# Kernel tuning notes

Hardware: AMD Instinct MI355X
Metric: run time of the kernel (lower is better)

## Reference

```python
import jax, jax.numpy as jnp
from jax import lax
import numpy as np

VOCAB, EMB = 50000, 300
HID, NCLS = 100, 20
BATCH, SEQ = 128, 512
P_DROP = 0.5


def setup_inputs() -> dict:
    key = jax.random.key(0)
    ks = jax.random.split(key, 8)
    s_e = 1.0 / np.sqrt(EMB)
    s_h = 1.0 / np.sqrt(HID)
    return {
        "inputs_batch": jax.random.randint(ks[0], (BATCH, SEQ), 0, VOCAB, dtype=jnp.int64)
        if jax.config.jax_enable_x64 else jax.random.randint(ks[0], (BATCH, SEQ), 0, VOCAB, dtype=jnp.int32),
        "emb_table": jax.random.normal(ks[1], (VOCAB, EMB), dtype=jnp.float32),
        # GRUCell params (torch layout): gates order [r, z, n]
        "w_ih": jax.random.uniform(ks[2], (3 * HID, EMB), jnp.float32, -s_h, s_h),
        "w_hh": jax.random.uniform(ks[3], (3 * HID, HID), jnp.float32, -s_h, s_h),
        "b_ih": jax.random.uniform(ks[4], (3 * HID,), jnp.float32, -s_h, s_h),
        "b_hh": jax.random.uniform(ks[5], (3 * HID,), jnp.float32, -s_h, s_h),
        "w_lin": jax.random.uniform(ks[6], (NCLS, HID), jnp.float32, -s_h, s_h),
        "b_lin": jax.random.uniform(ks[7], (NCLS,), jnp.float32, -s_h, s_h),
    }


def reference(inputs_batch, emb_table, w_ih, w_hh, b_ih, b_hh, w_lin, b_lin):
    B, S = inputs_batch.shape
    H = w_hh.shape[1]
    keep = 1.0 - P_DROP
    dk1, dk2 = jax.random.split(jax.random.key(42))

    z_embed = emb_table[inputs_batch]                       # [B, S, E]
    m1 = jax.random.bernoulli(dk1, keep, z_embed.shape)     # dropout1 mask
    z_embed = jnp.where(m1, z_embed / keep, 0.0)
    x_seq = jnp.swapaxes(z_embed, 0, 1)                     # [S, B, E]
    m2 = jax.random.bernoulli(dk2, keep, (S, B, H))         # per-step dropout2 masks

    def step(h, inp):
        x, m = inp
        gi = x @ w_ih.T + b_ih                              # [B, 3H]
        gh = h @ w_hh.T + b_hh
        i_r, i_z, i_n = jnp.split(gi, 3, axis=-1)
        h_r, h_z, h_n = jnp.split(gh, 3, axis=-1)
        r = jax.nn.sigmoid(i_r + h_r)
        zg = jax.nn.sigmoid(i_z + h_z)
        n = jnp.tanh(i_n + r * h_n)
        h_new = (1.0 - zg) * n + zg * h
        h_d = jnp.where(m, h_new / keep, 0.0)
        y = jax.nn.log_softmax(h_d @ w_lin.T + b_lin, axis=1)  # [B, C]
        return h_new, y

    h0 = jnp.zeros((B, H), dtype=x_seq.dtype)
    _, ys = lax.scan(step, h0, (x_seq, m2))                 # ys: [S, B, C]
    return jnp.transpose(ys, (1, 2, 0))                     # [B, C, S]
```

## Files before the change

kernel.cpp:

```cpp
#include <hip/hip_runtime.h>
#include <hip/hip_bf16.h>
#include <cstdint>

#define BATCH 128
#define SEQ   512
#define EMB   300
#define HID   100
#define G3    300
#define NCLS  20
#define NROWS (SEQ * BATCH)

#define M1_WORDS 614400
#define M2_WORDS 204800

typedef __attribute__((ext_vector_type(4))) float f32x4;
typedef __attribute__((ext_vector_type(8))) short s16x8;
typedef __fp16 h16x2 __attribute__((ext_vector_type(2)));

__host__ __device__ __forceinline__ void threefry2x32(uint32_t k0, uint32_t k1,
                                                      uint32_t x0, uint32_t x1,
                                                      uint32_t* o0, uint32_t* o1) {
  uint32_t ks2 = k0 ^ k1 ^ 0x1BD11BDAu;
  x0 += k0; x1 += k1;
#define TFR(r) { x0 += x1; x1 = (x1 << (r)) | (x1 >> (32 - (r))); x1 ^= x0; }
  TFR(13) TFR(15) TFR(26) TFR(6)  x0 += k1;  x1 += ks2 + 1u;
  TFR(17) TFR(29) TFR(16) TFR(24) x0 += ks2; x1 += k0 + 2u;
  TFR(13) TFR(15) TFR(26) TFR(6)  x0 += k0;  x1 += k1 + 3u;
  TFR(17) TFR(29) TFR(16) TFR(24) x0 += k1;  x1 += ks2 + 4u;
  TFR(13) TFR(15) TFR(26) TFR(6)  x0 += ks2; x1 += k0 + 5u;
#undef TFR
  *o0 = x0; *o1 = x1;
}

__device__ __forceinline__ uint32_t rand_bits32(uint32_t ka, uint32_t kb, uint32_t flat) {
  uint32_t a, b;
  threefry2x32(ka, kb, 0u, flat, &a, &b);
  return a ^ b;
}

__device__ __forceinline__ short f2bf(float f) {
  union { float f; uint32_t u; } c; c.f = f;
  uint32_t u = c.u;
  return (short)((u + 0x7FFFu + ((u >> 16) & 1u)) >> 16);
}

__device__ __forceinline__ void bar_lds() {
  __asm__ __volatile__("s_waitcnt lgkmcnt(0)" ::: "memory");
  __builtin_amdgcn_s_barrier();
  __asm__ __volatile__("" ::: "memory");
}

__device__ __forceinline__ float swz_xor4(float x) {
  return __builtin_bit_cast(float,
      __builtin_amdgcn_ds_swizzle(__builtin_bit_cast(int, x), 0x101F));
}

__global__ __launch_bounds__(256) void k_mask(uint32_t* __restrict__ M1w,
                                              uint32_t* __restrict__ M2w,
                                              uint32_t k1a, uint32_t k1b,
                                              uint32_t k2a, uint32_t k2b) {
  const int i = blockIdx.x * 256 + threadIdx.x;
  uint32_t ka, kb, base;
  uint32_t* dst;
  if (i < M1_WORDS) { ka = k1a; kb = k1b; base = (uint32_t)i * 32u; dst = M1w + i; }
  else { ka = k2a; kb = k2b; base = (uint32_t)(i - M1_WORDS) * 32u; dst = M2w + (i - M1_WORDS); }
  uint32_t w = 0u;
#pragma unroll
  for (int j = 0; j < 32; ++j) {
    uint32_t bits = rand_bits32(ka, kb, base + (uint32_t)j);
    w |= ((~bits) >> 31) << j;
  }
  *dst = w;
}

__global__ __launch_bounds__(256) void k_prepw(const float* __restrict__ w_ih,
                                               short* __restrict__ Wb) {
  int i8 = (blockIdx.x * 256 + threadIdx.x) * 8;
  if (i8 >= 304 * 320) return;
  short o[8];
#pragma unroll
  for (int j = 0; j < 8; ++j) {
    int pos = i8 + j;
    int n = pos / 320, k = pos - (pos / 320) * 320;
    float v = (n < 300 && k < 300) ? w_ih[(size_t)n * EMB + k] : 0.f;
    o[j] = f2bf(v);
  }
  *(s16x8*)(Wb + i8) = *(s16x8*)o;
}

__global__ __launch_bounds__(512) void k_gi7(const int* __restrict__ inputs,
                                             const float* __restrict__ emb,
                                             const short* __restrict__ Wb,
                                             const float* __restrict__ b_ih,
                                             const uint32_t* __restrict__ M1w,
                                             float* __restrict__ GI) {
  __shared__ short As[128 * 40];
  __shared__ short Bs[304 * 40];
  __shared__ int idxs[128];
  const int t = threadIdx.x;
  const int s = blockIdx.x;
  const int lane = t & 63, wave = t >> 6;
  const int wr = wave & 1;
  const int wc = wave >> 1;
  const int ml = lane & 15, quad = lane >> 4;
  const int arow = t >> 2;
  const int akq = t & 3;

  if (t < 128) idxs[t] = inputs[t * SEQ + s];
  __syncthreads();

  const int nfr = (wc < 3) ? 5 : 4;
  f32x4 acc[4][5];
#pragma unroll
  for (int i = 0; i < 4; ++i)
#pragma unroll
    for (int j = 0; j < 5; ++j) acc[i][j] = (f32x4){0.f, 0.f, 0.f, 0.f};

  const int myidx = idxs[arow];

  for (int c = 0; c < 10; ++c) {
    const int e0 = c * 32 + akq * 8;
    float xa[8];
#pragma unroll
    for (int j = 0; j < 8; ++j) xa[j] = 0.f;
    if (e0 + 7 < 300) {
#pragma unroll
      for (int q4 = 0; q4 < 2; ++q4) {
        float4 v = *(const float4*)(emb + (size_t)myidx * EMB + e0 + q4 * 4);
        xa[q4 * 4 + 0] = v.x; xa[q4 * 4 + 1] = v.y; xa[q4 * 4 + 2] = v.z; xa[q4 * 4 + 3] = v.w;
      }
    } else if (e0 < 300) {
#pragma unroll
      for (int j = 0; j < 8; ++j) {
        int e = e0 + j;
        if (e < 300) xa[j] = emb[(size_t)myidx * EMB + e];
      }
    }
    uint32_t mb = 0;
    if (e0 < 300) {
      uint32_t base = (uint32_t)((arow * SEQ + s) * EMB + e0);
      uint64_t mw = (uint64_t)M1w[base >> 5] | ((uint64_t)M1w[(base >> 5) + 1] << 32);
      mb = (uint32_t)(mw >> (base & 31));
    }
    short sa[8];
#pragma unroll
    for (int j = 0; j < 8; ++j)
      sa[j] = f2bf(((mb >> j) & 1u) ? xa[j] * 2.f : 0.f);
    s16x8 bv0, bv1, bv2;
    {
      int i0 = t;
      bv0 = *(const s16x8*)(Wb + (size_t)(i0 >> 2) * 320 + c * 32 + (i0 & 3) * 8);
      int i1 = t + 512;
      bv1 = *(const s16x8*)(Wb + (size_t)(i1 >> 2) * 320 + c * 32 + (i1 & 3) * 8);
      if (t < 192) {
        int i2 = t + 1024;
        bv2 = *(const s16x8*)(Wb + (size_t)(i2 >> 2) * 320 + c * 32 + (i2 & 3) * 8);
      }
    }
    if (c > 0) __syncthreads();
    *(s16x8*)&As[arow * 40 + akq * 8] = *(s16x8*)&sa[0];
    {
      int i0 = t;       *(s16x8*)&Bs[(i0 >> 2) * 40 + (i0 & 3) * 8] = bv0;
      int i1 = t + 512; *(s16x8*)&Bs[(i1 >> 2) * 40 + (i1 & 3) * 8] = bv1;
      if (t < 192) { int i2 = t + 1024; *(s16x8*)&Bs[(i2 >> 2) * 40 + (i2 & 3) * 8] = bv2; }
    }
    __syncthreads();
    s16x8 af[4];
#pragma unroll
    for (int mt = 0; mt < 4; ++mt)
      af[mt] = *(const s16x8*)&As[(wr * 64 + mt * 16 + ml) * 40 + quad * 8];
#pragma unroll
    for (int j = 0; j < 5; ++j) {
      if (j < nfr) {
        int nt = wc + 4 * j;
        s16x8 bf = *(const s16x8*)&Bs[(nt * 16 + ml) * 40 + quad * 8];
#pragma unroll
        for (int mt = 0; mt < 4; ++mt)
          acc[mt][j] = __builtin_amdgcn_mfma_f32_16x16x32_bf16(af[mt], bf, acc[mt][j], 0, 0, 0);
      }
    }
  }

#pragma unroll
  for (int j = 0; j < 5; ++j) {
    if (j < nfr) {
      int n = (wc + 4 * j) * 16 + ml;
      if (n < 300) {
        float bias = b_ih[n];
#pragma unroll
        for (int mt = 0; mt < 4; ++mt) {
#pragma unroll
          for (int i = 0; i < 4; ++i) {
            int brow = wr * 64 + mt * 16 + quad * 4 + i;
            GI[(size_t)(s * BATCH + brow) * G3 + n] = acc[mt][j][i] + bias;
          }
        }
      }
    }
  }
}

__global__ __launch_bounds__(512, 1) void k_rnn11(const float* __restrict__ GI,
                                                  const float* __restrict__ w_hh,
                                                  const float* __restrict__ b_hh,
                                                  const uint8_t* __restrict__ M2,
                                                  float* __restrict__ Hd) {
  __shared__ __align__(16) uint32_t hp_s[2][64];
  const int t = threadIdx.x, b = blockIdx.x;
  const int u = t >> 2, ks = t & 3;
  const bool act = (u < 100);
  const bool gate = act && (ks == 0);
  const int uc = act ? u : 99;
  const int kplo = (ks < 2) ? ks * 13 : 26 + (ks - 2) * 12;
  const int np = (ks < 2) ? 13 : 12;

  const float* rowR = w_hh + (size_t)uc * HID;
  const float* rowZ = w_hh + (size_t)(uc + 100) * HID;
  const float* rowN = w_hh + (size_t)(uc + 200) * HID;
  const h16x2 z2 = (h16x2){(__fp16)0.f, (__fp16)0.f};
  h16x2 wR[13], wZ[13], wN[13];
#pragma unroll
  for (int j = 0; j < 13; ++j) {
    if (j < np) {
      int o = 2 * (kplo + j);
      wR[j] = __builtin_amdgcn_cvt_pkrtz(rowR[o], rowR[o + 1]);
      wZ[j] = __builtin_amdgcn_cvt_pkrtz(rowZ[o], rowZ[o + 1]);
      wN[j] = __builtin_amdgcn_cvt_pkrtz(rowN[o], rowN[o + 1]);
    } else { wR[j] = z2; wZ[j] = z2; wN[j] = z2; }
  }

  float bR0 = 0.f, bZ0 = 0.f, bN0 = 0.f;
  float gcR = 0.f, gcZ = 0.f, gcN = 0.f;
  uint8_t mc = 0;
  if (gate) {
    bR0 = b_hh[u]; bZ0 = b_hh[100 + u]; bN0 = b_hh[200 + u];
    const float* g0 = GI + (size_t)b * G3;
    gcR = g0[u]; gcZ = g0[100 + u]; gcN = g0[200 + u];
    mc = M2[(uint32_t)(b * HID + u) >> 3];
  }
  const int p = u >> 1;
  const int sidx = (p < 13) ? 0 : (p < 26) ? 1 : (p < 38) ? 2 : 3;
  const int spos = p - ((sidx < 2) ? sidx * 13 : 26 + (sidx - 2) * 12);
  const int slot = sidx * 16 + spos;
  const bool writer = gate && !(u & 1);

  if (t < 128) ((uint32_t*)hp_s)[t] = 0u;
  float hprev = 0.f;
  __syncthreads();

#define QPX(x, c) __builtin_bit_cast(float, __builtin_amdgcn_mov_dpp( \
    __builtin_bit_cast(int, (x)), (c), 0xF, 0xF, true))
#define DOT1(J, W) { h16x2 hh = __builtin_bit_cast(h16x2, (W)); \
    sR = __builtin_amdgcn_fdot2(wR[J], hh, sR, false); \
    sZ = __builtin_amdgcn_fdot2(wZ[J], hh, sZ, false); \
    sN = __builtin_amdgcn_fdot2(wN[J], hh, sN, false); }

#pragma unroll 2
  for (int s = 0; s < SEQ; ++s) {
    float gnR = 0.f, gnZ = 0.f, gnN = 0.f;
    uint8_t mn = 0;
    if (gate) {
      int sn = (s + 1 < SEQ) ? s + 1 : s;
      const float* gp = GI + (size_t)(sn * BATCH + b) * G3;
      gnR = gp[u]; gnZ = gp[100 + u]; gnN = gp[200 + u];
      mn = M2[(uint32_t)((sn * BATCH + b) * HID + u) >> 3];
    }
    if (act) {
      float sR = bR0, sZ = bZ0, sN = bN0;
      const uint32_t* hb = &hp_s[s & 1][0] + (ks << 4);
      uint4 h0 = *(const uint4*)hb;
      uint4 h1 = *(const uint4*)(hb + 4);
      uint4 h2 = *(const uint4*)(hb + 8);
      uint32_t h3 = hb[12];
      DOT1(0, h0.x)  DOT1(1, h0.y)  DOT1(2, h0.z)  DOT1(3, h0.w)
      DOT1(4, h1.x)  DOT1(5, h1.y)  DOT1(6, h1.z)  DOT1(7, h1.w)
      DOT1(8, h2.x)  DOT1(9, h2.y)  DOT1(10, h2.z) DOT1(11, h2.w)
      DOT1(12, h3)
      sR += QPX(sR, 0xB1); sZ += QPX(sZ, 0xB1); sN += QPX(sN, 0xB1);
      sR += QPX(sR, 0x4E); sZ += QPX(sZ, 0x4E); sN += QPX(sN, 0x4E);
      if (gate) {
        float r = 1.f / (1.f + __expf(-(gcR + sR)));
        float z = 1.f / (1.f + __expf(-(gcZ + sZ)));
        float xn = gcN + r * sN;
        float e2 = __expf(2.f * fabsf(xn));
        float n = copysignf(1.f - 2.f / (e2 + 1.f), xn);
        float hnew = (1.f - z) * n + z * hprev;
        hprev = hnew;
        uint32_t fl = (uint32_t)((s * BATCH + b) * HID + u);
        float hd = ((mc >> (fl & 7)) & 1u) ? hnew * 2.f : 0.f;
        Hd[(size_t)(b * SEQ + s) * HID + u] = hd;
        float hoth = swz_xor4(hnew);
        if (writer)
          hp_s[(s & 1) ^ 1][slot] =
              __builtin_bit_cast(uint32_t, __builtin_amdgcn_cvt_pkrtz(hnew, hoth));
      }
    }
    gcR = gnR; gcZ = gnZ; gcN = gnN; mc = mn;
    bar_lds();
  }
#undef DOT1
#undef QPX
}

__global__ __launch_bounds__(64) void k_out(const float* __restrict__ Hd,
                                            const float* __restrict__ w_lin,
                                            const float* __restrict__ b_lin,
                                            float* __restrict__ out) {
  __shared__ float Wl[NCLS * HID];
  __shared__ float bl[NCLS];
  const int t = threadIdx.x;
  for (int i = t; i < NCLS * HID; i += 64) Wl[i] = w_lin[i];
  if (t < NCLS) bl[t] = b_lin[t];
  __syncthreads();

  const int r0 = (blockIdx.x * 64 + t) * 4;
  float acc[4][NCLS];
#pragma unroll
  for (int r = 0; r < 4; ++r)
#pragma unroll
    for (int c = 0; c < NCLS; ++c) acc[r][c] = bl[c];

  for (int k = 0; k < HID; k += 4) {
    float4 h0 = *(const float4*)(Hd + (size_t)(r0 + 0) * HID + k);
    float4 h1 = *(const float4*)(Hd + (size_t)(r0 + 1) * HID + k);
    float4 h2 = *(const float4*)(Hd + (size_t)(r0 + 2) * HID + k);
    float4 h3 = *(const float4*)(Hd + (size_t)(r0 + 3) * HID + k);
#pragma unroll
    for (int c = 0; c < NCLS; ++c) {
      float4 w4 = *(const float4*)&Wl[c * HID + k];
      acc[0][c] += h0.x * w4.x + h0.y * w4.y + h0.z * w4.z + h0.w * w4.w;
      acc[1][c] += h1.x * w4.x + h1.y * w4.y + h1.z * w4.z + h1.w * w4.w;
      acc[2][c] += h2.x * w4.x + h2.y * w4.y + h2.z * w4.z + h2.w * w4.w;
      acc[3][c] += h3.x * w4.x + h3.y * w4.y + h3.z * w4.z + h3.w * w4.w;
    }
  }

  float lse[4];
#pragma unroll
  for (int r = 0; r < 4; ++r) {
    float mx = acc[r][0];
#pragma unroll
    for (int c = 1; c < NCLS; ++c) mx = fmaxf(mx, acc[r][c]);
    float se = 0.f;
#pragma unroll
    for (int c = 0; c < NCLS; ++c) se += __expf(acc[r][c] - mx);
    lse[r] = mx + __logf(se);
  }
  const int b = r0 >> 9, s0 = r0 & 511;
#pragma unroll
  for (int c = 0; c < NCLS; ++c) {
    float4 o = make_float4(acc[0][c] - lse[0], acc[1][c] - lse[1],
                           acc[2][c] - lse[2], acc[3][c] - lse[3]);
    *(float4*)(out + (size_t)(b * NCLS + c) * SEQ + s0) = o;
  }
}

extern "C" void kernel_launch(void* const* d_in, const int* in_sizes, int n_in,
                              void* d_out, int out_size, void* d_ws, size_t ws_size,
                              hipStream_t stream) {
  const int*   inputs = (const int*)d_in[0];
  const float* emb    = (const float*)d_in[1];
  const float* w_ih   = (const float*)d_in[2];
  const float* w_hh   = (const float*)d_in[3];
  const float* b_ih   = (const float*)d_in[4];
  const float* b_hh   = (const float*)d_in[5];
  const float* w_lin  = (const float*)d_in[6];
  const float* b_lin  = (const float*)d_in[7];
  float* out = (float*)d_out;

  float* GI = (float*)d_ws;
  float* Hd = GI + (size_t)NROWS * G3;
  uint8_t* M1 = (uint8_t*)(Hd + (size_t)NROWS * HID);
  uint8_t* M2 = M1 + (size_t)M1_WORDS * 4;
  short* Wb = (short*)(M2 + (size_t)M2_WORDS * 4);

  uint32_t dk1a, dk1b, dk2a, dk2b;
  threefry2x32(0u, 42u, 0u, 0u, &dk1a, &dk1b);
  threefry2x32(0u, 42u, 0u, 1u, &dk2a, &dk2b);

  k_mask<<<(M1_WORDS + M2_WORDS) / 256, 256, 0, stream>>>(
      (uint32_t*)M1, (uint32_t*)M2, dk1a, dk1b, dk2a, dk2b);
  k_prepw<<<(304 * 320 / 8 + 255) / 256, 256, 0, stream>>>(w_ih, Wb);
  k_gi7<<<512, 512, 0, stream>>>(inputs, emb, Wb, b_ih, (const uint32_t*)M1, GI);
  k_rnn11<<<BATCH, 512, 0, stream>>>(GI, w_hh, b_hh, M2, Hd);
  k_out<<<256, 64, 0, stream>>>(Hd, w_lin, b_lin, out);
}
```

Baseline: 557.7 us.

## Split embedding gather and dropout into separate bf16 pre-pass before GI GEMM

```diff
diff --git a/kernel.cpp b/kernel.cpp
--- a/kernel.cpp
+++ b/kernel.cpp
@@ -86,6 +86,122 @@
     o[j] = f2bf(v);
   }
   *(s16x8*)(Wb + i8) = *(s16x8*)o;
+}
+
+__global__ __launch_bounds__(256) void k_prepx(const int* __restrict__ inputs,
+                                               const float* __restrict__ emb,
+                                               const uint32_t* __restrict__ M1w,
+                                               short* __restrict__ Xb) {
+  const int i8 = blockIdx.x * 256 + threadIdx.x;
+  const int r = i8 / 40, c8 = i8 - r * 40;
+  const int e = c8 * 8;
+  const int b = r & 127, sq = r >> 7;
+  short o[8];
+  if (e >= 300) {
+#pragma unroll
+    for (int j = 0; j < 8; ++j) o[j] = 0;
+  } else {
+    const int tok = inputs[b * SEQ + sq];
+    const float* er = emb + (size_t)tok * EMB + e;
+    float xa[8];
+    if (e + 8 <= 300) {
+      float4 v0 = *(const float4*)(er);
+      float4 v1 = *(const float4*)(er + 4);
+      xa[0] = v0.x; xa[1] = v0.y; xa[2] = v0.z; xa[3] = v0.w;
+      xa[4] = v1.x; xa[5] = v1.y; xa[6] = v1.z; xa[7] = v1.w;
+    } else {
+      float4 v0 = *(const float4*)(er);
+      xa[0] = v0.x; xa[1] = v0.y; xa[2] = v0.z; xa[3] = v0.w;
+      xa[4] = xa[5] = xa[6] = xa[7] = 0.f;
+    }
+    const uint32_t flat = (uint32_t)((b * SEQ + sq) * EMB + e);
+    uint64_t mw = (uint64_t)M1w[flat >> 5] | ((uint64_t)M1w[(flat >> 5) + 1] << 32);
+    uint32_t mb = (uint32_t)(mw >> (flat & 31));
+#pragma unroll
+    for (int j = 0; j < 8; ++j)
+      o[j] = f2bf(((mb >> j) & 1u) ? xa[j] * 2.f : 0.f);
+  }
+  *(s16x8*)(Xb + (size_t)i8 * 8) = *(s16x8*)o;
+}
+
+__global__ __launch_bounds__(512) void k_gi8(const short* __restrict__ Xb,
+                                             const short* __restrict__ Wb,
+                                             const float* __restrict__ b_ih,
+                                             float* __restrict__ GI) {
+  __shared__ short As[128 * 40];
+  __shared__ short Bs[304 * 40];
+  const int t = threadIdx.x;
+  const int s = blockIdx.x;
+  const int lane = t & 63, wave = t >> 6;
+  const int wr = wave & 1;
+  const int wc = wave >> 1;
+  const int ml = lane & 15, quad = lane >> 4;
+  const int arow = t >> 2;
+  const int akq = t & 3;
+
+  const int nfr = (wc < 3) ? 5 : 4;
+  f32x4 acc[4][5];
+#pragma unroll
+  for (int i = 0; i < 4; ++i)
+#pragma unroll
+    for (int j = 0; j < 5; ++j) acc[i][j] = (f32x4){0.f, 0.f, 0.f, 0.f};
+
+  const short* xrow = Xb + ((size_t)(s * 128) + arow) * 320;
+
+  for (int c = 0; c < 10; ++c) {
+    s16x8 av = *(const s16x8*)(xrow + c * 32 + akq * 8);
+    s16x8 bv0, bv1, bv2;
+    {
+      int i0 = t;
+      bv0 = *(const s16x8*)(Wb + (size_t)(i0 >> 2) * 320 + c * 32 + (i0 & 3) * 8);
+      int i1 = t + 512;
+      bv1 = *(const s16x8*)(Wb + (size_t)(i1 >> 2) * 320 + c * 32 + (i1 & 3) * 8);
+      if (t < 192) {
+        int i2 = t + 1024;
+        bv2 = *(const s16x8*)(Wb + (size_t)(i2 >> 2) * 320 + c * 32 + (i2 & 3) * 8);
+      }
+    }
+    if (c > 0) __syncthreads();
+    *(s16x8*)&As[arow * 40 + akq * 8] = av;
+    {
+      int i0 = t;       *(s16x8*)&Bs[(i0 >> 2) * 40 + (i0 & 3) * 8] = bv0;
+      int i1 = t + 512; *(s16x8*)&Bs[(i1 >> 2) * 40 + (i1 & 3) * 8] = bv1;
+      if (t < 192) { int i2 = t + 1024; *(s16x8*)&Bs[(i2 >> 2) * 40 + (i2 & 3) * 8] = bv2; }
+    }
+    __syncthreads();
+    s16x8 af[4];
+#pragma unroll
+    for (int mt = 0; mt < 4; ++mt)
+      af[mt] = *(const s16x8*)&As[(wr * 64 + mt * 16 + ml) * 40 + quad * 8];
+#pragma unroll
+    for (int j = 0; j < 5; ++j) {
+      if (j < nfr) {
+        int nt = wc + 4 * j;
+        s16x8 bf = *(const s16x8*)&Bs[(nt * 16 + ml) * 40 + quad * 8];
+#pragma unroll
+        for (int mt = 0; mt < 4; ++mt)
+          acc[mt][j] = __builtin_amdgcn_mfma_f32_16x16x32_bf16(af[mt], bf, acc[mt][j], 0, 0, 0);
+      }
+    }
+  }
+
+#pragma unroll
+  for (int j = 0; j < 5; ++j) {
+    if (j < nfr) {
+      int n = (wc + 4 * j) * 16 + ml;
+      if (n < 300) {
+        float bias = b_ih[n];
+#pragma unroll
+        for (int mt = 0; mt < 4; ++mt) {
+#pragma unroll
+          for (int i = 0; i < 4; ++i) {
+            int brow = wr * 64 + mt * 16 + quad * 4 + i;
+            GI[(size_t)(s * BATCH + brow) * G3 + n] = acc[mt][j][i] + bias;
+          }
+        }
+      }
+    }
+  }
 }
 
 __global__ __launch_bounds__(512) void k_gi7(const int* __restrict__ inputs,
@@ -265,6 +381,7 @@
       gnR = gp[u]; gnZ = gp[100 + u]; gnN = gp[200 + u];
       mn = M2[(uint32_t)((sn * BATCH + b) * HID + u) >> 3];
     }
+
     if (act) {
       float sR = bR0, sZ = bZ0, sN = bN0;
       const uint32_t* hb = &hp_s[s & 1][0] + (ks << 4);
@@ -287,7 +404,7 @@
         float hnew = (1.f - z) * n + z * hprev;
         hprev = hnew;
         uint32_t fl = (uint32_t)((s * BATCH + b) * HID + u);
-        float hd = ((mc >> (fl & 7)) & 1u) ? hnew * 2.f : 0.f;
+        float hd = ((mc >> (fl & 7)) & 1) ? hnew * 2.f : 0.f;
         Hd[(size_t)(b * SEQ + s) * HID + u] = hd;
         float hoth = swz_xor4(hnew);
         if (writer)
@@ -373,6 +490,8 @@
   uint8_t* M1 = (uint8_t*)(Hd + (size_t)NROWS * HID);
   uint8_t* M2 = M1 + (size_t)M1_WORDS * 4;
   short* Wb = (short*)(M2 + (size_t)M2_WORDS * 4);
+  short* Xb = Wb + 304 * 320;
+  const size_t need_xb = 150272000;
 
   uint32_t dk1a, dk1b, dk2a, dk2b;
   threefry2x32(0u, 42u, 0u, 0u, &dk1a, &dk1b);
@@ -381,7 +500,13 @@
   k_mask<<<(M1_WORDS + M2_WORDS) / 256, 256, 0, stream>>>(
       (uint32_t*)M1, (uint32_t*)M2, dk1a, dk1b, dk2a, dk2b);
   k_prepw<<<(304 * 320 / 8 + 255) / 256, 256, 0, stream>>>(w_ih, Wb);
-  k_gi7<<<512, 512, 0, stream>>>(inputs, emb, Wb, b_ih, (const uint32_t*)M1, GI);
+  if (ws_size >= need_xb) {
+    k_prepx<<<65536 * 40 / 256, 256, 0, stream>>>(inputs, emb,
+                                                  (const uint32_t*)M1, Xb);
+    k_gi8<<<512, 512, 0, stream>>>(Xb, Wb, b_ih, GI);
+  } else {
+    k_gi7<<<512, 512, 0, stream>>>(inputs, emb, Wb, b_ih, (const uint32_t*)M1, GI);
+  }
   k_rnn11<<<BATCH, 512, 0, stream>>>(GI, w_hh, b_hh, M2, Hd);
   k_out<<<256, 64, 0, stream>>>(Hd, w_lin, b_lin, out);
 }
```

New measurement: 559.4 us. About the same (+0.3%).

## Fuse input projection, GRU recurrence and output head into one per-batch kernel

Applied to the files above, without the earlier changes.

```diff
diff --git a/kernel.cpp b/kernel.cpp
--- a/kernel.cpp
+++ b/kernel.cpp
@@ -55,198 +55,209 @@
       __builtin_amdgcn_ds_swizzle(__builtin_bit_cast(int, x), 0x101F));
 }
 
-__global__ __launch_bounds__(256) void k_mask(uint32_t* __restrict__ M1w,
+__global__ __launch_bounds__(256) void k_prep(uint32_t* __restrict__ M1w,
                                               uint32_t* __restrict__ M2w,
+                                              const float* __restrict__ w_ih,
+                                              short* __restrict__ Wb,
                                               uint32_t k1a, uint32_t k1b,
                                               uint32_t k2a, uint32_t k2b) {
-  const int i = blockIdx.x * 256 + threadIdx.x;
-  uint32_t ka, kb, base;
-  uint32_t* dst;
-  if (i < M1_WORDS) { ka = k1a; kb = k1b; base = (uint32_t)i * 32u; dst = M1w + i; }
-  else { ka = k2a; kb = k2b; base = (uint32_t)(i - M1_WORDS) * 32u; dst = M2w + (i - M1_WORDS); }
-  uint32_t w = 0u;
-#pragma unroll
-  for (int j = 0; j < 32; ++j) {
-    uint32_t bits = rand_bits32(ka, kb, base + (uint32_t)j);
-    w |= ((~bits) >> 31) << j;
+  const int bid = blockIdx.x;
+  if (bid < 3200) {
+    const int i = bid * 256 + threadIdx.x;
+    uint32_t ka, kb, base;
+    uint32_t* dst;
+    if (i < M1_WORDS) { ka = k1a; kb = k1b; base = (uint32_t)i * 32u; dst = M1w + i; }
+    else { ka = k2a; kb = k2b; base = (uint32_t)(i - M1_WORDS) * 32u; dst = M2w + (i - M1_WORDS); }
+    uint32_t w = 0u;
+#pragma unroll
+    for (int j = 0; j < 32; ++j) {
+      uint32_t bits = rand_bits32(ka, kb, base + (uint32_t)j);
+      w |= ((~bits) >> 31) << j;
+    }
+    *dst = w;
+  } else {
+    int i8 = ((bid - 3200) * 256 + threadIdx.x) * 8;
+    if (i8 >= 304 * 320) return;
+    short o[8];
+#pragma unroll
+    for (int j = 0; j < 8; ++j) {
+      int pos = i8 + j;
+      int n = pos / 320, k = pos - (pos / 320) * 320;
+      float v = (n < 300 && k < 300) ? w_ih[(size_t)n * EMB + k] : 0.f;
+      o[j] = f2bf(v);
+    }
+    *(s16x8*)(Wb + i8) = *(s16x8*)o;
   }
-  *dst = w;
-}
-
-__global__ __launch_bounds__(256) void k_prepw(const float* __restrict__ w_ih,
-                                               short* __restrict__ Wb) {
-  int i8 = (blockIdx.x * 256 + threadIdx.x) * 8;
-  if (i8 >= 304 * 320) return;
-  short o[8];
-#pragma unroll
-  for (int j = 0; j < 8; ++j) {
-    int pos = i8 + j;
-    int n = pos / 320, k = pos - (pos / 320) * 320;
-    float v = (n < 300 && k < 300) ? w_ih[(size_t)n * EMB + k] : 0.f;
-    o[j] = f2bf(v);
+}
+
+__global__ __launch_bounds__(512, 1) void k_main(const int* __restrict__ inputs,
+                                                 const float* __restrict__ emb,
+                                                 const short* __restrict__ Wb,
+                                                 const float* __restrict__ b_ih,
+                                                 const uint32_t* __restrict__ M1w,
+                                                 float* __restrict__ GI,
+                                                 const float* __restrict__ w_hh,
+                                                 const float* __restrict__ b_hh,
+                                                 const uint8_t* __restrict__ M2,
+                                                 float* __restrict__ Hd,
+                                                 const float* __restrict__ w_lin,
+                                                 const float* __restrict__ b_lin,
+                                                 float* __restrict__ out) {
+  __shared__ __align__(16) char smem[35072];
+  const int t = threadIdx.x, b = blockIdx.x;
+  float* GIb = GI + (size_t)b * SEQ * G3;
+
+  {
+    short* As = (short*)smem;
+    short* Bs = As + 128 * 40;
+    int* idxs = (int*)(Bs + 304 * 40);
+    const int lane = t & 63, wave = t >> 6;
+    const int wr = wave & 1, wc = wave >> 1;
+    const int ml = lane & 15, quad = lane >> 4;
+    const int arow = t >> 2, akq = t & 3;
+    const int nfr = (wc < 3) ? 5 : 4;
+
+    for (int tile = 0; tile < 4; ++tile) {
+      __syncthreads();
+      if (t < 128) idxs[t] = inputs[b * SEQ + tile * 128 + t];
+      __syncthreads();
+
+      f32x4 acc[4][5];
+#pragma unroll
+      for (int i = 0; i < 4; ++i)
+#pragma unroll
+        for (int j = 0; j < 5; ++j) acc[i][j] = (f32x4){0.f, 0.f, 0.f, 0.f};
+
+      const int myidx = idxs[arow];
+      const int srow = tile * 128 + arow;
+
+      for (int c = 0; c < 10; ++c) {
+        const int e0 = c * 32 + akq * 8;
+        float xa[8];
+#pragma unroll
+        for (int j = 0; j < 8; ++j) xa[j] = 0.f;
+        if (e0 + 7 < 300) {
+#pragma unroll
+          for (int q4 = 0; q4 < 2; ++q4) {
+            float4 v = *(const float4*)(emb + (size_t)myidx * EMB + e0 + q4 * 4);
+            xa[q4 * 4 + 0] = v.x; xa[q4 * 4 + 1] = v.y;
+            xa[q4 * 4 + 2] = v.z; xa[q4 * 4 + 3] = v.w;
+          }
+        } else if (e0 < 300) {
+#pragma unroll
+          for (int j = 0; j < 8; ++j) {
+            int e = e0 + j;
+            if (e < 300) xa[j] = emb[(size_t)myidx * EMB + e];
+          }
+        }
+        uint32_t mb = 0;
+        if (e0 < 300) {
+          uint32_t base = (uint32_t)((b * SEQ + srow) * EMB + e0);
+          uint64_t mw = (uint64_t)M1w[base >> 5] | ((uint64_t)M1w[(base >> 5) + 1] << 32);
+          mb = (uint32_t)(mw >> (base & 31));
+        }
+        short sa[8];
+#pragma unroll
+        for (int j = 0; j < 8; ++j)
+          sa[j] = f2bf(((mb >> j) & 1u) ? xa[j] * 2.f : 0.f);
+        s16x8 bv0, bv1, bv2;
+        {
+          int i0 = t;
+          bv0 = *(const s16x8*)(Wb + (size_t)(i0 >> 2) * 320 + c * 32 + (i0 & 3) * 8);
+          int i1 = t + 512;
+          bv1 = *(const s16x8*)(Wb + (size_t)(i1 >> 2) * 320 + c * 32 + (i1 & 3) * 8);
+          if (t < 192) {
+            int i2 = t + 1024;
+            bv2 = *(const s16x8*)(Wb + (size_t)(i2 >> 2) * 320 + c * 32 + (i2 & 3) * 8);
+          }
+        }
+        if (c > 0) __syncthreads();
+        *(s16x8*)&As[arow * 40 + akq * 8] = *(s16x8*)&sa[0];
+        {
+          int i0 = t;       *(s16x8*)&Bs[(i0 >> 2) * 40 + (i0 & 3) * 8] = bv0;
+          int i1 = t + 512; *(s16x8*)&Bs[(i1 >> 2) * 40 + (i1 & 3) * 8] = bv1;
+          if (t < 192) { int i2 = t + 1024; *(s16x8*)&Bs[(i2 >> 2) * 40 + (i2 & 3) * 8] = bv2; }
+        }
+        __syncthreads();
+        s16x8 af[4];
+#pragma unroll
+        for (int mt = 0; mt < 4; ++mt)
+          af[mt] = *(const s16x8*)&As[(wr * 64 + mt * 16 + ml) * 40 + quad * 8];
+#pragma unroll
+        for (int j = 0; j < 5; ++j) {
+          if (j < nfr) {
+            int nt = wc + 4 * j;
+            s16x8 bf = *(const s16x8*)&Bs[(nt * 16 + ml) * 40 + quad * 8];
+#pragma unroll
+            for (int mt = 0; mt < 4; ++mt)
+              acc[mt][j] = __builtin_amdgcn_mfma_f32_16x16x32_bf16(af[mt], bf, acc[mt][j], 0, 0, 0);
+          }
+        }
+      }
+
+#pragma unroll
+      for (int j = 0; j < 5; ++j) {
+        if (j < nfr) {
+          int n = (wc + 4 * j) * 16 + ml;
+          if (n < 300) {
+            float bias = b_ih[n];
+#pragma unroll
+            for (int mt = 0; mt < 4; ++mt) {
+#pragma unroll
+              for (int i = 0; i < 4; ++i) {
+                int so = tile * 128 + wr * 64 + mt * 16 + quad * 4 + i;
+                GIb[(size_t)so * G3 + n] = acc[mt][j][i] + bias;
+              }
+            }
+          }
+        }
+      }
+    }
   }
-  *(s16x8*)(Wb + i8) = *(s16x8*)o;
-}
-
-__global__ __launch_bounds__(512) void k_gi7(const int* __restrict__ inputs,
-                                             const float* __restrict__ emb,
-                                             const short* __restrict__ Wb,
-                                             const float* __restrict__ b_ih,
-                                             const uint32_t* __restrict__ M1w,
-                                             float* __restrict__ GI) {
-  __shared__ short As[128 * 40];
-  __shared__ short Bs[304 * 40];
-  __shared__ int idxs[128];
-  const int t = threadIdx.x;
-  const int s = blockIdx.x;
-  const int lane = t & 63, wave = t >> 6;
-  const int wr = wave & 1;
-  const int wc = wave >> 1;
-  const int ml = lane & 15, quad = lane >> 4;
-  const int arow = t >> 2;
-  const int akq = t & 3;
-
-  if (t < 128) idxs[t] = inputs[t * SEQ + s];
+  __threadfence_block();
   __syncthreads();
 
-  const int nfr = (wc < 3) ? 5 : 4;
-  f32x4 acc[4][5];
-#pragma unroll
-  for (int i = 0; i < 4; ++i)
-#pragma unroll
-    for (int j = 0; j < 5; ++j) acc[i][j] = (f32x4){0.f, 0.f, 0.f, 0.f};
-
-  const int myidx = idxs[arow];
-
-  for (int c = 0; c < 10; ++c) {
-    const int e0 = c * 32 + akq * 8;
-    float xa[8];
-#pragma unroll
-    for (int j = 0; j < 8; ++j) xa[j] = 0.f;
-    if (e0 + 7 < 300) {
-#pragma unroll
-      for (int q4 = 0; q4 < 2; ++q4) {
-        float4 v = *(const float4*)(emb + (size_t)myidx * EMB + e0 + q4 * 4);
-        xa[q4 * 4 + 0] = v.x; xa[q4 * 4 + 1] = v.y; xa[q4 * 4 + 2] = v.z; xa[q4 * 4 + 3] = v.w;
-      }
-    } else if (e0 < 300) {
-#pragma unroll
-      for (int j = 0; j < 8; ++j) {
-        int e = e0 + j;
-        if (e < 300) xa[j] = emb[(size_t)myidx * EMB + e];
-      }
-    }
-    uint32_t mb = 0;
-    if (e0 < 300) {
-      uint32_t base = (uint32_t)((arow * SEQ + s) * EMB + e0);
-      uint64_t mw = (uint64_t)M1w[base >> 5] | ((uint64_t)M1w[(base >> 5) + 1] << 32);
-      mb = (uint32_t)(mw >> (base & 31));
-    }
-    short sa[8];
-#pragma unroll
-    for (int j = 0; j < 8; ++j)
-      sa[j] = f2bf(((mb >> j) & 1u) ? xa[j] * 2.f : 0.f);
-    s16x8 bv0, bv1, bv2;
-    {
-      int i0 = t;
-      bv0 = *(const s16x8*)(Wb + (size_t)(i0 >> 2) * 320 + c * 32 + (i0 & 3) * 8);
-      int i1 = t + 512;
-      bv1 = *(const s16x8*)(Wb + (size_t)(i1 >> 2) * 320 + c * 32 + (i1 & 3) * 8);
-      if (t < 192) {
-        int i2 = t + 1024;
-        bv2 = *(const s16x8*)(Wb + (size_t)(i2 >> 2) * 320 + c * 32 + (i2 & 3) * 8);
-      }
-    }
-    if (c > 0) __syncthreads();
-    *(s16x8*)&As[arow * 40 + akq * 8] = *(s16x8*)&sa[0];
-    {
-      int i0 = t;       *(s16x8*)&Bs[(i0 >> 2) * 40 + (i0 & 3) * 8] = bv0;
-      int i1 = t + 512; *(s16x8*)&Bs[(i1 >> 2) * 40 + (i1 & 3) * 8] = bv1;
-      if (t < 192) { int i2 = t + 1024; *(s16x8*)&Bs[(i2 >> 2) * 40 + (i2 & 3) * 8] = bv2; }
-    }
+  {
+    uint32_t (*hp_s)[64] = (uint32_t (*)[64])smem;
+    const int u = t >> 2, ks = t & 3;
+    const bool act = (u < 100);
+    const bool gate = act && (ks == 0);
+    const int uc = act ? u : 99;
+    const int kplo = (ks < 2) ? ks * 13 : 26 + (ks - 2) * 12;
+    const int np = (ks < 2) ? 13 : 12;
+
+    const float* rowR = w_hh + (size_t)uc * HID;
+    const float* rowZ = w_hh + (size_t)(uc + 100) * HID;
+    const float* rowN = w_hh + (size_t)(uc + 200) * HID;
+    const h16x2 z2 = (h16x2){(__fp16)0.f, (__fp16)0.f};
+    h16x2 wR[13], wZ[13], wN[13];
+#pragma unroll
+    for (int j = 0; j < 13; ++j) {
+      if (j < np) {
+        int o = 2 * (kplo + j);
+        wR[j] = __builtin_amdgcn_cvt_pkrtz(rowR[o], rowR[o + 1]);
+        wZ[j] = __builtin_amdgcn_cvt_pkrtz(rowZ[o], rowZ[o + 1]);
+        wN[j] = __builtin_amdgcn_cvt_pkrtz(rowN[o], rowN[o + 1]);
+      } else { wR[j] = z2; wZ[j] = z2; wN[j] = z2; }
+    }
+
+    float bR0 = 0.f, bZ0 = 0.f, bN0 = 0.f;
+    float gcR = 0.f, gcZ = 0.f, gcN = 0.f;
+    uint8_t mc = 0;
+    if (gate) {
+      bR0 = b_hh[u]; bZ0 = b_hh[100 + u]; bN0 = b_hh[200 + u];
+      gcR = GIb[u]; gcZ = GIb[100 + u]; gcN = GIb[200 + u];
+      mc = M2[(uint32_t)(b * HID + u) >> 3];
+    }
+    const int p = u >> 1;
+    const int sidx = (p < 13) ? 0 : (p < 26) ? 1 : (p < 38) ? 2 : 3;
+    const int spos = p - ((sidx < 2) ? sidx * 13 : 26 + (sidx - 2) * 12);
+    const int slot = sidx * 16 + spos;
+    const bool writer = gate && !(u & 1);
+
+    if (t < 128) ((uint32_t*)hp_s)[t] = 0u;
+    float hprev = 0.f;
     __syncthreads();
-    s16x8 af[4];
-#pragma unroll
-    for (int mt = 0; mt < 4; ++mt)
-      af[mt] = *(const s16x8*)&As[(wr * 64 + mt * 16 + ml) * 40 + quad * 8];
-#pragma unroll
-    for (int j = 0; j < 5; ++j) {
-      if (j < nfr) {
-        int nt = wc + 4 * j;
-        s16x8 bf = *(const s16x8*)&Bs[(nt * 16 + ml) * 40 + quad * 8];
-#pragma unroll
-        for (int mt = 0; mt < 4; ++mt)
-          acc[mt][j] = __builtin_amdgcn_mfma_f32_16x16x32_bf16(af[mt], bf, acc[mt][j], 0, 0, 0);
-      }
-    }
-  }
-
-#pragma unroll
-  for (int j = 0; j < 5; ++j) {
-    if (j < nfr) {
-      int n = (wc + 4 * j) * 16 + ml;
-      if (n < 300) {
-        float bias = b_ih[n];
-#pragma unroll
-        for (int mt = 0; mt < 4; ++mt) {
-#pragma unroll
-          for (int i = 0; i < 4; ++i) {
-            int brow = wr * 64 + mt * 16 + quad * 4 + i;
-            GI[(size_t)(s * BATCH + brow) * G3 + n] = acc[mt][j][i] + bias;
-          }
-        }
-      }
-    }
-  }
-}
-
-__global__ __launch_bounds__(512, 1) void k_rnn11(const float* __restrict__ GI,
-                                                  const float* __restrict__ w_hh,
-                                                  const float* __restrict__ b_hh,
-                                                  const uint8_t* __restrict__ M2,
-                                                  float* __restrict__ Hd) {
-  __shared__ __align__(16) uint32_t hp_s[2][64];
-  const int t = threadIdx.x, b = blockIdx.x;
-  const int u = t >> 2, ks = t & 3;
-  const bool act = (u < 100);
-  const bool gate = act && (ks == 0);
-  const int uc = act ? u : 99;
-  const int kplo = (ks < 2) ? ks * 13 : 26 + (ks - 2) * 12;
-  const int np = (ks < 2) ? 13 : 12;
-
-  const float* rowR = w_hh + (size_t)uc * HID;
-  const float* rowZ = w_hh + (size_t)(uc + 100) * HID;
-  const float* rowN = w_hh + (size_t)(uc + 200) * HID;
-  const h16x2 z2 = (h16x2){(__fp16)0.f, (__fp16)0.f};
-  h16x2 wR[13], wZ[13], wN[13];
-#pragma unroll
-  for (int j = 0; j < 13; ++j) {
-    if (j < np) {
-      int o = 2 * (kplo + j);
-      wR[j] = __builtin_amdgcn_cvt_pkrtz(rowR[o], rowR[o + 1]);
-      wZ[j] = __builtin_amdgcn_cvt_pkrtz(rowZ[o], rowZ[o + 1]);
-      wN[j] = __builtin_amdgcn_cvt_pkrtz(rowN[o], rowN[o + 1]);
-    } else { wR[j] = z2; wZ[j] = z2; wN[j] = z2; }
-  }
-
-  float bR0 = 0.f, bZ0 = 0.f, bN0 = 0.f;
-  float gcR = 0.f, gcZ = 0.f, gcN = 0.f;
-  uint8_t mc = 0;
-  if (gate) {
-    bR0 = b_hh[u]; bZ0 = b_hh[100 + u]; bN0 = b_hh[200 + u];
-    const float* g0 = GI + (size_t)b * G3;
-    gcR = g0[u]; gcZ = g0[100 + u]; gcN = g0[200 + u];
-    mc = M2[(uint32_t)(b * HID + u) >> 3];
-  }
-  const int p = u >> 1;
-  const int sidx = (p < 13) ? 0 : (p < 26) ? 1 : (p < 38) ? 2 : 3;
-  const int spos = p - ((sidx < 2) ? sidx * 13 : 26 + (sidx - 2) * 12);
-  const int slot = sidx * 16 + spos;
-  const bool writer = gate && !(u & 1);
-
-  if (t < 128) ((uint32_t*)hp_s)[t] = 0u;
-  float hprev = 0.f;
-  __syncthreads();
 
 #define QPX(x, c) __builtin_bit_cast(float, __builtin_amdgcn_mov_dpp( \
     __builtin_bit_cast(int, (x)), (c), 0xF, 0xF, true))
@@ -256,102 +267,84 @@
     sN = __builtin_amdgcn_fdot2(wN[J], hh, sN, false); }
 
 #pragma unroll 2
-  for (int s = 0; s < SEQ; ++s) {
-    float gnR = 0.f, gnZ = 0.f, gnN = 0.f;
-    uint8_t mn = 0;
-    if (gate) {
-      int sn = (s + 1 < SEQ) ? s + 1 : s;
-      const float* gp = GI + (size_t)(sn * BATCH + b) * G3;
-      gnR = gp[u]; gnZ = gp[100 + u]; gnN = gp[200 + u];
-      mn = M2[(uint32_t)((sn * BATCH + b) * HID + u) >> 3];
-    }
-    if (act) {
-      float sR = bR0, sZ = bZ0, sN = bN0;
-      const uint32_t* hb = &hp_s[s & 1][0] + (ks << 4);
-      uint4 h0 = *(const uint4*)hb;
-      uint4 h1 = *(const uint4*)(hb + 4);
-      uint4 h2 = *(const uint4*)(hb + 8);
-      uint32_t h3 = hb[12];
-      DOT1(0, h0.x)  DOT1(1, h0.y)  DOT1(2, h0.z)  DOT1(3, h0.w)
-      DOT1(4, h1.x)  DOT1(5, h1.y)  DOT1(6, h1.z)  DOT1(7, h1.w)
-      DOT1(8, h2.x)  DOT1(9, h2.y)  DOT1(10, h2.z) DOT1(11, h2.w)
-      DOT1(12, h3)
-      sR += QPX(sR, 0xB1); sZ += QPX(sZ, 0xB1); sN += QPX(sN, 0xB1);
-      sR += QPX(sR, 0x4E); sZ += QPX(sZ, 0x4E); sN += QPX(sN, 0x4E);
+    for (int s = 0; s < SEQ; ++s) {
+      float gnR = 0.f, gnZ = 0.f, gnN = 0.f;
+      uint8_t mn = 0;
       if (gate) {
-        float r = 1.f / (1.f + __expf(-(gcR + sR)));
-        float z = 1.f / (1.f + __expf(-(gcZ + sZ)));
-        float xn = gcN + r * sN;
-        float e2 = __expf(2.f * fabsf(xn));
-        float n = copysignf(1.f - 2.f / (e2 + 1.f), xn);
-        float hnew = (1.f - z) * n + z * hprev;
-        hprev = hnew;
-        uint32_t fl = (uint32_t)((s * BATCH + b) * HID + u);
-        float hd = ((mc >> (fl & 7)) & 1u) ? hnew * 2.f : 0.f;
-        Hd[(size_t)(b * SEQ + s) * HID + u] = hd;
-        float hoth = swz_xor4(hnew);
-        if (writer)
-          hp_s[(s & 1) ^ 1][slot] =
-              __builtin_bit_cast(uint32_t, __builtin_amdgcn_cvt_pkrtz(hnew, hoth));
-      }
-    }
-    gcR = gnR; gcZ = gnZ; gcN = gnN; mc = mn;
-    bar_lds();
-  }
+        int sn = (s + 1 < SEQ) ? s + 1 : s;
+        const float* gp = GIb + (size_t)sn * G3;
+        gnR = gp[u]; gnZ = gp[100 + u]; gnN = gp[200 + u];
+        mn = M2[(uint32_t)((sn * BATCH + b) * HID + u) >> 3];
+      }
+
+      if (act) {
+        float sR = bR0, sZ = bZ0, sN = bN0;
+        const uint32_t* hb = &hp_s[s & 1][0] + (ks << 4);
+        uint4 h0 = *(const uint4*)hb;
+        uint4 h1 = *(const uint4*)(hb + 4);
+        uint4 h2 = *(const uint4*)(hb + 8);
+        uint32_t h3 = hb[12];
+        DOT1(0, h0.x)  DOT1(1, h0.y)  DOT1(2, h0.z)  DOT1(3, h0.w)
+        DOT1(4, h1.x)  DOT1(5, h1.y)  DOT1(6, h1.z)  DOT1(7, h1.w)
+        DOT1(8, h2.x)  DOT1(9, h2.y)  DOT1(10, h2.z) DOT1(11, h2.w)
+        DOT1(12, h3)
+        sR += QPX(sR, 0xB1); sZ += QPX(sZ, 0xB1); sN += QPX(sN, 0xB1);
+        sR += QPX(sR, 0x4E); sZ += QPX(sZ, 0x4E); sN += QPX(sN, 0x4E);
+        if (gate) {
+          float r = 1.f / (1.f + __expf(-(gcR + sR)));
+          float z = 1.f / (1.f + __expf(-(gcZ + sZ)));
+          float xn = gcN + r * sN;
+          float e2 = __expf(2.f * fabsf(xn));
+          float n = copysignf(1.f - 2.f / (e2 + 1.f), xn);
+          float hnew = (1.f - z) * n + z * hprev;
+          hprev = hnew;
+          uint32_t fl = (uint32_t)((s * BATCH + b) * HID + u);
+          float hd = ((mc >> (fl & 7)) & 1) ? hnew * 2.f : 0.f;
+          Hd[(size_t)(b * SEQ + s) * HID + u] = hd;
+          float hoth = swz_xor4(hnew);
+          if (writer)
+            hp_s[(s & 1) ^ 1][slot] =
+                __builtin_bit_cast(uint32_t, __builtin_amdgcn_cvt_pkrtz(hnew, hoth));
+        }
+      }
+      gcR = gnR; gcZ = gnZ; gcN = gnN; mc = mn;
+      bar_lds();
+    }
 #undef DOT1
 #undef QPX
-}
-
-__global__ __launch_bounds__(64) void k_out(const float* __restrict__ Hd,
-                                            const float* __restrict__ w_lin,
-                                            const float* __restrict__ b_lin,
-                                            float* __restrict__ out) {
-  __shared__ float Wl[NCLS * HID];
-  __shared__ float bl[NCLS];
-  const int t = threadIdx.x;
-  for (int i = t; i < NCLS * HID; i += 64) Wl[i] = w_lin[i];
-  if (t < NCLS) bl[t] = b_lin[t];
-  __syncthreads();
-
-  const int r0 = (blockIdx.x * 64 + t) * 4;
-  float acc[4][NCLS];
-#pragma unroll
-  for (int r = 0; r < 4; ++r)
-#pragma unroll
-    for (int c = 0; c < NCLS; ++c) acc[r][c] = bl[c];
-
-  for (int k = 0; k < HID; k += 4) {
-    float4 h0 = *(const float4*)(Hd + (size_t)(r0 + 0) * HID + k);
-    float4 h1 = *(const float4*)(Hd + (size_t)(r0 + 1) * HID + k);
-    float4 h2 = *(const float4*)(Hd + (size_t)(r0 + 2) * HID + k);
-    float4 h3 = *(const float4*)(Hd + (size_t)(r0 + 3) * HID + k);
-#pragma unroll
-    for (int c = 0; c < NCLS; ++c) {
-      float4 w4 = *(const float4*)&Wl[c * HID + k];
-      acc[0][c] += h0.x * w4.x + h0.y * w4.y + h0.z * w4.z + h0.w * w4.w;
-      acc[1][c] += h1.x * w4.x + h1.y * w4.y + h1.z * w4.z + h1.w * w4.w;
-      acc[2][c] += h2.x * w4.x + h2.y * w4.y + h2.z * w4.z + h2.w * w4.w;
-      acc[3][c] += h3.x * w4.x + h3.y * w4.y + h3.z * w4.z + h3.w * w4.w;
-    }
   }
 
-  float lse[4];
-#pragma unroll
-  for (int r = 0; r < 4; ++r) {
-    float mx = acc[r][0];
-#pragma unroll
-    for (int c = 1; c < NCLS; ++c) mx = fmaxf(mx, acc[r][c]);
+  {
+    float* Wl = (float*)smem;
+    float* bl = Wl + NCLS * HID;
+    __syncthreads();
+    for (int i = t; i < NCLS * HID; i += 512) Wl[i] = w_lin[i];
+    if (t < NCLS) bl[t] = b_lin[t];
+    __syncthreads();
+
+    const int s = t;
+    const float* hrow = Hd + ((size_t)b * SEQ + s) * HID;
+    float acc[NCLS];
+#pragma unroll
+    for (int c = 0; c < NCLS; ++c) acc[c] = bl[c];
+    for (int k = 0; k < HID; k += 4) {
+      const float4 h = *(const float4*)(hrow + k);
+#pragma unroll
+      for (int c = 0; c < NCLS; ++c) {
+        const float4 w4 = *(const float4*)&Wl[c * HID + k];
+        acc[c] += h.x * w4.x + h.y * w4.y + h.z * w4.z + h.w * w4.w;
+      }
+    }
+    float mx = acc[0];
+#pragma unroll
+    for (int c = 1; c < NCLS; ++c) mx = fmaxf(mx, acc[c]);
     float se = 0.f;
 #pragma unroll
-    for (int c = 0; c < NCLS; ++c) se += __expf(acc[r][c] - mx);
-    lse[r] = mx + __logf(se);
-  }
-  const int b = r0 >> 9, s0 = r0 & 511;
-#pragma unroll
-  for (int c = 0; c < NCLS; ++c) {
-    float4 o = make_float4(acc[0][c] - lse[0], acc[1][c] - lse[1],
-                           acc[2][c] - lse[2], acc[3][c] - lse[3]);
-    *(float4*)(out + (size_t)(b * NCLS + c) * SEQ + s0) = o;
+    for (int c = 0; c < NCLS; ++c) se += __expf(acc[c] - mx);
+    const float lse = mx + __logf(se);
+#pragma unroll
+    for (int c = 0; c < NCLS; ++c)
+      out[(size_t)(b * NCLS + c) * SEQ + s] = acc[c] - lse;
   }
 }
 
@@ -378,10 +371,8 @@
   threefry2x32(0u, 42u, 0u, 0u, &dk1a, &dk1b);
   threefry2x32(0u, 42u, 0u, 1u, &dk2a, &dk2b);
 
-  k_mask<<<(M1_WORDS + M2_WORDS) / 256, 256, 0, stream>>>(
-      (uint32_t*)M1, (uint32_t*)M2, dk1a, dk1b, dk2a, dk2b);
-  k_prepw<<<(304 * 320 / 8 + 255) / 256, 256, 0, stream>>>(w_ih, Wb);
-  k_gi7<<<512, 512, 0, stream>>>(inputs, emb, Wb, b_ih, (const uint32_t*)M1, GI);
-  k_rnn11<<<BATCH, 512, 0, stream>>>(GI, w_hh, b_hh, M2, Hd);
-  k_out<<<256, 64, 0, stream>>>(Hd, w_lin, b_lin, out);
-}
+  k_prep<<<3248, 256, 0, stream>>>((uint32_t*)M1, (uint32_t*)M2, w_ih, Wb,
+                                   dk1a, dk1b, dk2a, dk2b);
+  k_main<<<BATCH, 512, 0, stream>>>(inputs, emb, Wb, b_ih, (const uint32_t*)M1,
+                                    GI, w_hh, b_hh, M2, Hd, w_lin, b_lin, out);
+}
```

Measured after the change: 553.0 us. No clear change (-0.9%).
